# Kernel optimization log

Measured on AMD Instinct MI355X. Metric: run time of the kernel, lower is better.

Reference implementation:

```python
import jax, jax.numpy as jnp
import numpy as np

N_SRC, N_TGT, K = 16384, 65536, 8      # coarse nodes, fine nodes, IDW neighbours per target
C, C_SKIP, S, HID = 16, 2, 32, 64      # mv channels (d_model), skip mv channels, scalars, MLP hidden
MV = 16                                # PGA multivector blade dimension


def setup_inputs() -> dict:
    key = jax.random.key(0)
    ks = jax.random.split(key, 11)
    E = N_TGT * K
    return {
        'mv_src': jax.random.normal(ks[0], (N_SRC, C, MV), jnp.float32),
        'mv_skip': jax.random.normal(ks[1], (N_TGT, C_SKIP, MV), jnp.float32),
        'sc_src': jax.random.normal(ks[2], (N_SRC, S), jnp.float32),
        'sc_skip': jax.random.normal(ks[3], (N_TGT, S), jnp.float32),
        'pos_src': jax.random.uniform(ks[4], (N_SRC, 3), jnp.float32),
        'pos_tgt': jax.random.uniform(ks[5], (N_TGT, 3), jnp.float32),
        'interp_source': jax.random.randint(ks[6], (E,), 0, N_SRC, dtype=jnp.int32),
        # every target receives exactly K source contributions (sorted, like torch_geometric knn edges)
        'interp_target': jnp.repeat(jnp.arange(N_TGT, dtype=jnp.int32), K),
        'W1_mv': jax.random.normal(ks[7], (C + C_SKIP, HID), jnp.float32) / np.float32(np.sqrt(C + C_SKIP)),
        'W2_mv': jax.random.normal(ks[8], (HID, C), jnp.float32) / np.float32(np.sqrt(HID)),
        'W1_s': jax.random.normal(ks[9], (2 * S, HID), jnp.float32) / np.float32(np.sqrt(2 * S)),
        'b1_s': jnp.zeros((HID,), jnp.float32),
        'W2_s': jax.random.normal(ks[10], (HID, S), jnp.float32) / np.float32(np.sqrt(HID)),
        'b2_s': jnp.zeros((S,), jnp.float32),
    }


def _interp(mv_src, mv_skip, sc_src, sc_skip, pos_src, pos_tgt,
            interp_source, interp_target, W1_mv, W2_mv, W1_s, b1_s, W2_s, b2_s):
    # --- inverse-distance-weighted interpolation (gather -> weight -> scatter-sum) ---
    pos_diff = pos_src[interp_source] - pos_tgt[interp_target]            # [E,3]
    d2 = jnp.clip(jnp.sum(pos_diff * pos_diff, axis=-1), 1e-16)           # [E]
    w = 1.0 / d2                                                          # IDW weight
    denom = jax.ops.segment_sum(w, interp_target, num_segments=N_TGT)     # [N_tgt]
    mv = jax.ops.segment_sum(mv_src[interp_source] * w[:, None, None],
                             interp_target, num_segments=N_TGT) / denom[:, None, None]
    sc = jax.ops.segment_sum(sc_src[interp_source] * w[:, None],
                             interp_target, num_segments=N_TGT) / denom[:, None]
    # --- skip concat (torch.cat dim=-2 for multivectors, dim=-1 for scalars) ---
    mv = jnp.concatenate((mv, mv_skip), axis=-2)                          # [N_tgt, C+C_SKIP, 16]
    sc = jnp.concatenate((sc, sc_skip), axis=-1)                          # [N_tgt, 2S]
    # --- equivariant MLP: channel-mixing linear on multivectors (blade-wise), gated scalar path ---
    mv_h = jnp.einsum('nci,ch->nhi', mv, W1_mv)                           # [N_tgt, HID, 16]
    sc_h = jax.nn.gelu(sc @ W1_s + b1_s)                                  # [N_tgt, HID]
    mv_o = jnp.einsum('nhi,hc->nci', mv_h, W2_mv)                         # [N_tgt, C, 16]
    sc_o = sc_h @ W2_s + b2_s                                             # [N_tgt, S]
    return mv_o, sc_o


def reference(mv_src, mv_skip, sc_src, sc_skip, pos_src, pos_tgt,
              interp_source, interp_target, W1_mv, W2_mv, W1_s, b1_s, W2_s, b2_s):
    return _interp(mv_src, mv_skip, sc_src, sc_skip, pos_src, pos_tgt,
                   interp_source, interp_target, W1_mv, W2_mv, W1_s, b1_s, W2_s, b2_s)
```

## Files before the change

kernel.cpp:

```cpp
#include <hip/hip_runtime.h>

#define N_SRC 16384
#define N_TGT 65536
#define KNN 8
#define CMV 16
#define CSKIP 2
#define SSC 32
#define HID 64
#define MVD 16

#define OUT_MV_ELEMS (N_TGT * CMV * MVD)
#define PROJ_OFFSET 512

__device__ __forceinline__ float gelu_tanh(float x) {
    const float k0 = 0.7978845608028654f;
    const float k1 = 0.044715f;
    float y = k0 * fmaf(k1 * x, x * x * x >= 0.f ? x * x : x * x, x);
    (void)y;
    float yy = k0 * (x + k1 * x * x * x);
    return 0.5f * x * (1.0f + tanhf(yy));
}

__global__ __launch_bounds__(256) void kA_preproject(
        const float* __restrict__ mv_src,
        const float* __restrict__ W1_mv,
        const float* __restrict__ W2_mv,
        float* __restrict__ ws) {
    __shared__ float sWeff[CMV][MVD];
    int tid = threadIdx.x;
    {
        int c = tid >> 4, d = tid & 15;
        float a = 0.f;
        #pragma unroll 8
        for (int h = 0; h < HID; ++h)
            a = fmaf(W1_mv[c * HID + h], W2_mv[h * MVD + d], a);
        sWeff[c][d] = a;
    }
    if (blockIdx.x == 0 && tid < 32) {
        int j = tid >> 4, d = tid & 15;
        float a = 0.f;
        #pragma unroll 8
        for (int h = 0; h < HID; ++h)
            a = fmaf(W1_mv[(CMV + j) * HID + h], W2_mv[h * MVD + d], a);
        ws[j * MVD + d] = a;
    }
    __syncthreads();

    int lane = tid & 63;
    int d = lane >> 2, q = lane & 3;
    float wcol[CMV];
    #pragma unroll
    for (int c = 0; c < CMV; ++c) wcol[c] = sWeff[c][d];

    float* proj = ws + PROJ_OFFSET;
    int wid = (int)((blockIdx.x * blockDim.x + tid) >> 6);
    int nw  = (int)((gridDim.x * blockDim.x) >> 6);
    for (int s = wid; s < N_SRC; s += nw) {
        const float* row = mv_src + (size_t)s * 256;
        float4 o = make_float4(0.f, 0.f, 0.f, 0.f);
        #pragma unroll
        for (int c = 0; c < CMV; ++c) {
            float4 v = *(const float4*)(row + c * 16 + q * 4);
            o.x = fmaf(v.x, wcol[c], o.x);
            o.y = fmaf(v.y, wcol[c], o.y);
            o.z = fmaf(v.z, wcol[c], o.z);
            o.w = fmaf(v.w, wcol[c], o.w);
        }
        *(float4*)(proj + (size_t)s * 256 + lane * 4) = o;
    }
}

__global__ __launch_bounds__(256) void kB_mv(
        const float* __restrict__ ws,
        const float* __restrict__ mv_skip,
        const float* __restrict__ pos_src,
        const float* __restrict__ pos_tgt,
        const int*   __restrict__ isrc,
        float* __restrict__ out) {
    int tid = threadIdx.x;
    int lane = tid & 63;
    int d = lane >> 2, q = lane & 3;
    float wsk0 = ws[d];
    float wsk1 = ws[MVD + d];
    const float* proj = ws + PROJ_OFFSET;

    int wid = (int)((blockIdx.x * blockDim.x + tid) >> 6);
    int nw  = (int)((gridDim.x * blockDim.x) >> 6);
    for (int t = wid; t < N_TGT; t += nw) {
        float w = 0.f; int src = 0;
        if (lane < KNN) {
            src = isrc[t * KNN + lane];
            float dx = pos_src[src * 3 + 0] - pos_tgt[t * 3 + 0];
            float dy = pos_src[src * 3 + 1] - pos_tgt[t * 3 + 1];
            float dz = pos_src[src * 3 + 2] - pos_tgt[t * 3 + 2];
            float d2 = fmaxf(dx * dx + dy * dy + dz * dz, 1e-16f);
            w = 1.0f / d2;
        }
        float denom = w;
        denom += __shfl_xor(denom, 1);
        denom += __shfl_xor(denom, 2);
        denom += __shfl_xor(denom, 4);
        denom = __shfl(denom, 0);
        float invd = 1.0f / denom;

        float4 acc = make_float4(0.f, 0.f, 0.f, 0.f);
        #pragma unroll
        for (int k = 0; k < KNN; ++k) {
            int   sk = __builtin_amdgcn_readlane(src, k);
            float wk = __uint_as_float(__builtin_amdgcn_readlane(__float_as_uint(w), k));
            float4 v = *(const float4*)(proj + (size_t)sk * 256 + lane * 4);
            acc.x = fmaf(wk, v.x, acc.x);
            acc.y = fmaf(wk, v.y, acc.y);
            acc.z = fmaf(wk, v.z, acc.z);
            acc.w = fmaf(wk, v.w, acc.w);
        }
        const float4 u0 = *(const float4*)(mv_skip + (size_t)t * 32 + q * 4);
        const float4 u1 = *(const float4*)(mv_skip + (size_t)t * 32 + 16 + q * 4);
        float4 o;
        o.x = fmaf(acc.x, invd, fmaf(wsk0, u0.x, wsk1 * u1.x));
        o.y = fmaf(acc.y, invd, fmaf(wsk0, u0.y, wsk1 * u1.y));
        o.z = fmaf(acc.z, invd, fmaf(wsk0, u0.z, wsk1 * u1.z));
        o.w = fmaf(acc.w, invd, fmaf(wsk0, u0.w, wsk1 * u1.w));
        *(float4*)(out + (size_t)t * 256 + lane * 4) = o;
    }
}

__global__ __launch_bounds__(256) void kBf_mv(
        const float* __restrict__ mv_src,
        const float* __restrict__ mv_skip,
        const float* __restrict__ pos_src,
        const float* __restrict__ pos_tgt,
        const int*   __restrict__ isrc,
        const float* __restrict__ W1_mv,
        const float* __restrict__ W2_mv,
        float* __restrict__ out) {
    __shared__ float sWeff[CMV + CSKIP][MVD];
    __shared__ float stage[4][256];
    int tid = threadIdx.x;
    for (int e = tid; e < (CMV + CSKIP) * MVD; e += 256) {
        int c = e >> 4, d = e & 15;
        float a = 0.f;
        #pragma unroll 8
        for (int h = 0; h < HID; ++h)
            a = fmaf(W1_mv[c * HID + h], W2_mv[h * MVD + d], a);
        sWeff[c][d] = a;
    }
    __syncthreads();

    int lane = tid & 63, wv = tid >> 6;
    int d = lane >> 2, q = lane & 3;
    float wcol[CMV + CSKIP];
    #pragma unroll
    for (int c = 0; c < CMV + CSKIP; ++c) wcol[c] = sWeff[c][d];

    int wid = (int)((blockIdx.x * blockDim.x + tid) >> 6);
    int nw  = (int)((gridDim.x * blockDim.x) >> 6);
    for (int t = wid; t < N_TGT; t += nw) {
        float w = 0.f; int src = 0;
        if (lane < KNN) {
            src = isrc[t * KNN + lane];
            float dx = pos_src[src * 3 + 0] - pos_tgt[t * 3 + 0];
            float dy = pos_src[src * 3 + 1] - pos_tgt[t * 3 + 1];
            float dz = pos_src[src * 3 + 2] - pos_tgt[t * 3 + 2];
            float d2 = fmaxf(dx * dx + dy * dy + dz * dz, 1e-16f);
            w = 1.0f / d2;
        }
        float denom = w;
        denom += __shfl_xor(denom, 1);
        denom += __shfl_xor(denom, 2);
        denom += __shfl_xor(denom, 4);
        denom = __shfl(denom, 0);
        float invd = 1.0f / denom;

        float4 acc = make_float4(0.f, 0.f, 0.f, 0.f);
        #pragma unroll
        for (int k = 0; k < KNN; ++k) {
            int   sk = __builtin_amdgcn_readlane(src, k);
            float wk = __uint_as_float(__builtin_amdgcn_readlane(__float_as_uint(w), k));
            float4 v = *(const float4*)(mv_src + (size_t)sk * 256 + lane * 4);
            acc.x = fmaf(wk, v.x, acc.x);
            acc.y = fmaf(wk, v.y, acc.y);
            acc.z = fmaf(wk, v.z, acc.z);
            acc.w = fmaf(wk, v.w, acc.w);
        }
        asm volatile("" ::: "memory");
        *(float4*)&stage[wv][lane * 4] = acc;
        asm volatile("s_waitcnt lgkmcnt(0)" ::: "memory");
        __builtin_amdgcn_sched_barrier(0);

        float4 o = make_float4(0.f, 0.f, 0.f, 0.f);
        #pragma unroll
        for (int c = 0; c < CMV; ++c) {
            float4 v = *(const float4*)&stage[wv][c * 16 + q * 4];
            o.x = fmaf(v.x, wcol[c], o.x);
            o.y = fmaf(v.y, wcol[c], o.y);
            o.z = fmaf(v.z, wcol[c], o.z);
            o.w = fmaf(v.w, wcol[c], o.w);
        }
        const float4 u0 = *(const float4*)(mv_skip + (size_t)t * 32 + q * 4);
        const float4 u1 = *(const float4*)(mv_skip + (size_t)t * 32 + 16 + q * 4);
        float4 r;
        r.x = fmaf(o.x, invd, fmaf(wcol[16], u0.x, wcol[17] * u1.x));
        r.y = fmaf(o.y, invd, fmaf(wcol[16], u0.y, wcol[17] * u1.y));
        r.z = fmaf(o.z, invd, fmaf(wcol[16], u0.z, wcol[17] * u1.z));
        r.w = fmaf(o.w, invd, fmaf(wcol[16], u0.w, wcol[17] * u1.w));
        *(float4*)(out + (size_t)t * 256 + lane * 4) = r;
    }
}

__global__ __launch_bounds__(256) void kC_scalar(
        const float* __restrict__ sc_src,
        const float* __restrict__ sc_skip,
        const float* __restrict__ pos_src,
        const float* __restrict__ pos_tgt,
        const int*   __restrict__ isrc,
        const float* __restrict__ W1_s,
        const float* __restrict__ b1_s,
        const float* __restrict__ W2_s,
        const float* __restrict__ b2_s,
        float* __restrict__ out) {
    __shared__ float sW1[HID * HID];
    __shared__ float sW2T[SSC][68];
    __shared__ float sXT[HID][64];
    __shared__ float sH[64][68];
    __shared__ float swgt[64][9];
    __shared__ int   ssrcl[64][9];
    __shared__ float sb1[HID], sb2[SSC];

    int tid = threadIdx.x;
    #pragma unroll
    for (int r = 0; r < 4; ++r) {
        float4 v = *(const float4*)(W1_s + (r * 256 + tid) * 4);
        *(float4*)&sW1[(r * 256 + tid) * 4] = v;
    }
    for (int e = tid; e < HID * SSC; e += 256) {
        int h = e >> 5, s = e & 31;
        sW2T[s][h] = W2_s[e];
    }
    if (tid < HID) sb1[tid] = b1_s[tid];
    else if (tid < HID + SSC) sb2[tid - HID] = b2_s[tid - HID];

    int t0 = blockIdx.x * 64;
    if (tid < 64) {
        int t = t0 + tid;
        float ptx = pos_tgt[t * 3 + 0], pty = pos_tgt[t * 3 + 1], ptz = pos_tgt[t * 3 + 2];
        int4 e0 = *(const int4*)(isrc + t * KNN);
        int4 e1 = *(const int4*)(isrc + t * KNN + 4);
        int sk[KNN] = {e0.x, e0.y, e0.z, e0.w, e1.x, e1.y, e1.z, e1.w};
        float wk[KNN];
        float denom = 0.f;
        #pragma unroll
        for (int k = 0; k < KNN; ++k) {
            int s = sk[k];
            float dx = pos_src[s * 3 + 0] - ptx;
            float dy = pos_src[s * 3 + 1] - pty;
            float dz = pos_src[s * 3 + 2] - ptz;
            float d2 = fmaxf(dx * dx + dy * dy + dz * dz, 1e-16f);
            wk[k] = 1.0f / d2;
            denom += wk[k];
        }
        float invd = 1.0f / denom;
        #pragma unroll
        for (int k = 0; k < KNN; ++k) {
            swgt[tid][k] = wk[k] * invd;
            ssrcl[tid][k] = sk[k];
        }
    }
    __syncthreads();

    {
        int tl = tid & 63;
        int part = tid >> 6;
        float cat[16];
        if (part < 2) {
            #pragma unroll
            for (int i = 0; i < 16; ++i) cat[i] = 0.f;
            #pragma unroll
            for (int k = 0; k < KNN; ++k) {
                float wn = swgt[tl][k];
                const float* row = sc_src + (size_t)ssrcl[tl][k] * SSC + part * 16;
                #pragma unroll
                for (int i4 = 0; i4 < 4; ++i4) {
                    float4 v = *(const float4*)(row + i4 * 4);
                    cat[i4 * 4 + 0] = fmaf(wn, v.x, cat[i4 * 4 + 0]);
                    cat[i4 * 4 + 1] = fmaf(wn, v.y, cat[i4 * 4 + 1]);
                    cat[i4 * 4 + 2] = fmaf(wn, v.z, cat[i4 * 4 + 2]);
                    cat[i4 * 4 + 3] = fmaf(wn, v.w, cat[i4 * 4 + 3]);
                }
            }
        } else {
            const float* row = sc_skip + (size_t)(t0 + tl) * SSC + (part - 2) * 16;
            #pragma unroll
            for (int i4 = 0; i4 < 4; ++i4) {
                float4 v = *(const float4*)(row + i4 * 4);
                cat[i4 * 4 + 0] = v.x; cat[i4 * 4 + 1] = v.y;
                cat[i4 * 4 + 2] = v.z; cat[i4 * 4 + 3] = v.w;
            }
        }
        #pragma unroll
        for (int i = 0; i < 16; ++i)
            sXT[part * 16 + i][tl] = cat[i];
    }
    __syncthreads();

    int wv = tid >> 6;
    int lane = tid & 63;
    int tr4 = lane >> 4;
    int hc  = lane & 15;
    int tbase = wv * 16 + tr4 * 4;
    float acc[4][4];
    #pragma unroll
    for (int i = 0; i < 4; ++i)
        #pragma unroll
        for (int j = 0; j < 4; ++j) acc[i][j] = 0.f;

    #pragma unroll 2
    for (int c = 0; c < HID; ++c) {
        float4 xv = *(const float4*)&sXT[c][tbase];
        float4 wv4 = *(const float4*)&sW1[c * HID + hc * 4];
        acc[0][0] = fmaf(xv.x, wv4.x, acc[0][0]);
        acc[0][1] = fmaf(xv.x, wv4.y, acc[0][1]);
        acc[0][2] = fmaf(xv.x, wv4.z, acc[0][2]);
        acc[0][3] = fmaf(xv.x, wv4.w, acc[0][3]);
        acc[1][0] = fmaf(xv.y, wv4.x, acc[1][0]);
        acc[1][1] = fmaf(xv.y, wv4.y, acc[1][1]);
        acc[1][2] = fmaf(xv.y, wv4.z, acc[1][2]);
        acc[1][3] = fmaf(xv.y, wv4.w, acc[1][3]);
        acc[2][0] = fmaf(xv.z, wv4.x, acc[2][0]);
        acc[2][1] = fmaf(xv.z, wv4.y, acc[2][1]);
        acc[2][2] = fmaf(xv.z, wv4.z, acc[2][2]);
        acc[2][3] = fmaf(xv.z, wv4.w, acc[2][3]);
        acc[3][0] = fmaf(xv.w, wv4.x, acc[3][0]);
        acc[3][1] = fmaf(xv.w, wv4.y, acc[3][1]);
        acc[3][2] = fmaf(xv.w, wv4.z, acc[3][2]);
        acc[3][3] = fmaf(xv.w, wv4.w, acc[3][3]);
    }
    {
        float b0 = sb1[hc * 4 + 0], b1 = sb1[hc * 4 + 1];
        float b2 = sb1[hc * 4 + 2], b3 = sb1[hc * 4 + 3];
        #pragma unroll
        for (int i = 0; i < 4; ++i) {
            float4 hv;
            hv.x = gelu_tanh(acc[i][0] + b0);
            hv.y = gelu_tanh(acc[i][1] + b1);
            hv.z = gelu_tanh(acc[i][2] + b2);
            hv.w = gelu_tanh(acc[i][3] + b3);
            *(float4*)&sH[tbase + i][hc * 4] = hv;
        }
    }
    __syncthreads();

    int sc16 = lane & 15;
    float acc2[4][2];
    #pragma unroll
    for (int i = 0; i < 4; ++i) { acc2[i][0] = 0.f; acc2[i][1] = 0.f; }
    #pragma unroll 2
    for (int hh = 0; hh < 16; ++hh) {
        float4 wa = *(const float4*)&sW2T[sc16 * 2 + 0][hh * 4];
        float4 wb = *(const float4*)&sW2T[sc16 * 2 + 1][hh * 4];
        #pragma unroll
        for (int i = 0; i < 4; ++i) {
            float4 hv = *(const float4*)&sH[tbase + i][hh * 4];
            acc2[i][0] = fmaf(hv.x, wa.x, acc2[i][0]);
            acc2[i][0] = fmaf(hv.y, wa.y, acc2[i][0]);
            acc2[i][0] = fmaf(hv.z, wa.z, acc2[i][0]);
            acc2[i][0] = fmaf(hv.w, wa.w, acc2[i][0]);
            acc2[i][1] = fmaf(hv.x, wb.x, acc2[i][1]);
            acc2[i][1] = fmaf(hv.y, wb.y, acc2[i][1]);
            acc2[i][1] = fmaf(hv.z, wb.z, acc2[i][1]);
            acc2[i][1] = fmaf(hv.w, wb.w, acc2[i][1]);
        }
    }
    float* osc = out + OUT_MV_ELEMS;
    float bb0 = sb2[sc16 * 2 + 0], bb1 = sb2[sc16 * 2 + 1];
    #pragma unroll
    for (int i = 0; i < 4; ++i) {
        int t = t0 + tbase + i;
        float2 r = make_float2(acc2[i][0] + bb0, acc2[i][1] + bb1);
        *(float2*)&osc[(size_t)t * SSC + sc16 * 2] = r;
    }
}

extern "C" void kernel_launch(void* const* d_in, const int* in_sizes, int n_in,
                              void* d_out, int out_size, void* d_ws, size_t ws_size,
                              hipStream_t stream) {
    const float* mv_src   = (const float*)d_in[0];
    const float* mv_skip  = (const float*)d_in[1];
    const float* sc_src   = (const float*)d_in[2];
    const float* sc_skip  = (const float*)d_in[3];
    const float* pos_src  = (const float*)d_in[4];
    const float* pos_tgt  = (const float*)d_in[5];
    const int*   isrc     = (const int*)d_in[6];
    const float* W1_mv    = (const float*)d_in[8];
    const float* W2_mv    = (const float*)d_in[9];
    const float* W1_s     = (const float*)d_in[10];
    const float* b1_s     = (const float*)d_in[11];
    const float* W2_s     = (const float*)d_in[12];
    const float* b2_s     = (const float*)d_in[13];
    float* out = (float*)d_out;
    float* ws  = (float*)d_ws;

    size_t need_ws_bytes = (size_t)(PROJ_OFFSET + (size_t)N_SRC * 256) * sizeof(float);
    if (ws_size >= need_ws_bytes) {
        hipLaunchKernelGGL(kA_preproject, dim3(512), dim3(256), 0, stream,
                           mv_src, W1_mv, W2_mv, ws);
        hipLaunchKernelGGL(kB_mv, dim3(2048), dim3(256), 0, stream,
                           ws, mv_skip, pos_src, pos_tgt, isrc, out);
    } else {
        hipLaunchKernelGGL(kBf_mv, dim3(2048), dim3(256), 0, stream,
                           mv_src, mv_skip, pos_src, pos_tgt, isrc, W1_mv, W2_mv, out);
    }
    hipLaunchKernelGGL(kC_scalar, dim3(N_TGT / 64), dim3(256), 0, stream,
                       sc_src, sc_skip, pos_src, pos_tgt, isrc,
                       W1_s, b1_s, W2_s, b2_s, out);
}
```

Measured before the change: 234.7 us.

## Batch 8 targets per wave and gather sources in phase order for L2 locality

Measured after the change: 238.4 us. About the same (+1.6%).

```diff
diff --git a/kernel.cpp b/kernel.cpp
--- a/kernel.cpp
+++ b/kernel.cpp
@@ -12,11 +12,12 @@
 #define OUT_MV_ELEMS (N_TGT * CMV * MVD)
 #define PROJ_OFFSET 512
 
+#define NPHASE 8
+#define PSHIFT 11
+
 __device__ __forceinline__ float gelu_tanh(float x) {
     const float k0 = 0.7978845608028654f;
     const float k1 = 0.044715f;
-    float y = k0 * fmaf(k1 * x, x * x * x >= 0.f ? x * x : x * x, x);
-    (void)y;
     float yy = k0 * (x + k1 * x * x * x);
     return 0.5f * x * (1.0f + tanhf(yy));
 }
@@ -85,42 +86,64 @@
     const float* proj = ws + PROJ_OFFSET;
 
     int wid = (int)((blockIdx.x * blockDim.x + tid) >> 6);
-    int nw  = (int)((gridDim.x * blockDim.x) >> 6);
-    for (int t = wid; t < N_TGT; t += nw) {
-        float w = 0.f; int src = 0;
+    int t0 = wid * 8;
+
+    int   srcv[8];
+    float wnv[8];
+    #pragma unroll
+    for (int tl = 0; tl < 8; ++tl) {
+        int t = t0 + tl;
+        float w = 0.f; int s = 0;
         if (lane < KNN) {
-            src = isrc[t * KNN + lane];
-            float dx = pos_src[src * 3 + 0] - pos_tgt[t * 3 + 0];
-            float dy = pos_src[src * 3 + 1] - pos_tgt[t * 3 + 1];
-            float dz = pos_src[src * 3 + 2] - pos_tgt[t * 3 + 2];
+            s = isrc[t * KNN + lane];
+            float dx = pos_src[s * 3 + 0] - pos_tgt[t * 3 + 0];
+            float dy = pos_src[s * 3 + 1] - pos_tgt[t * 3 + 1];
+            float dz = pos_src[s * 3 + 2] - pos_tgt[t * 3 + 2];
             float d2 = fmaxf(dx * dx + dy * dy + dz * dz, 1e-16f);
             w = 1.0f / d2;
         }
-        float denom = w;
-        denom += __shfl_xor(denom, 1);
-        denom += __shfl_xor(denom, 2);
-        denom += __shfl_xor(denom, 4);
-        denom = __shfl(denom, 0);
-        float invd = 1.0f / denom;
-
-        float4 acc = make_float4(0.f, 0.f, 0.f, 0.f);
-        #pragma unroll
-        for (int k = 0; k < KNN; ++k) {
-            int   sk = __builtin_amdgcn_readlane(src, k);
-            float wk = __uint_as_float(__builtin_amdgcn_readlane(__float_as_uint(w), k));
-            float4 v = *(const float4*)(proj + (size_t)sk * 256 + lane * 4);
-            acc.x = fmaf(wk, v.x, acc.x);
-            acc.y = fmaf(wk, v.y, acc.y);
-            acc.z = fmaf(wk, v.z, acc.z);
-            acc.w = fmaf(wk, v.w, acc.w);
-        }
+        float den = w;
+        den += __shfl_xor(den, 1);
+        den += __shfl_xor(den, 2);
+        den += __shfl_xor(den, 4);
+        srcv[tl] = s;
+        wnv[tl]  = w / den;
+    }
+
+    float4 acc[8];
+    #pragma unroll
+    for (int tl = 0; tl < 8; ++tl) acc[tl] = make_float4(0.f, 0.f, 0.f, 0.f);
+
+    for (int p = 0; p < NPHASE; ++p) {
+        #pragma unroll
+        for (int tl = 0; tl < 8; ++tl) {
+            unsigned long long m =
+                __ballot((lane < KNN) && ((srcv[tl] >> PSHIFT) == p));
+            while (m) {
+                int k = __builtin_ctzll(m);
+                m &= m - 1;
+                int   sk = __builtin_amdgcn_readlane(srcv[tl], k);
+                float wk = __uint_as_float(
+                    __builtin_amdgcn_readlane(__float_as_uint(wnv[tl]), k));
+                const float4 v = *(const float4*)(proj + (size_t)sk * 256 + lane * 4);
+                acc[tl].x = fmaf(wk, v.x, acc[tl].x);
+                acc[tl].y = fmaf(wk, v.y, acc[tl].y);
+                acc[tl].z = fmaf(wk, v.z, acc[tl].z);
+                acc[tl].w = fmaf(wk, v.w, acc[tl].w);
+            }
+        }
+    }
+
+    #pragma unroll
+    for (int tl = 0; tl < 8; ++tl) {
+        int t = t0 + tl;
         const float4 u0 = *(const float4*)(mv_skip + (size_t)t * 32 + q * 4);
         const float4 u1 = *(const float4*)(mv_skip + (size_t)t * 32 + 16 + q * 4);
         float4 o;
-        o.x = fmaf(acc.x, invd, fmaf(wsk0, u0.x, wsk1 * u1.x));
-        o.y = fmaf(acc.y, invd, fmaf(wsk0, u0.y, wsk1 * u1.y));
-        o.z = fmaf(acc.z, invd, fmaf(wsk0, u0.z, wsk1 * u1.z));
-        o.w = fmaf(acc.w, invd, fmaf(wsk0, u0.w, wsk1 * u1.w));
+        o.x = acc[tl].x + fmaf(wsk0, u0.x, wsk1 * u1.x);
+        o.y = acc[tl].y + fmaf(wsk0, u0.y, wsk1 * u1.y);
+        o.z = acc[tl].z + fmaf(wsk0, u0.z, wsk1 * u1.z);
+        o.w = acc[tl].w + fmaf(wsk0, u0.w, wsk1 * u1.w);
         *(float4*)(out + (size_t)t * 256 + lane * 4) = o;
     }
 }
```

## Store pre-projected source multivectors in fp16 and batch target gathers

Applied to the files above, without the earlier changes.

Measured after the change: 208.6 us. -11.1%, faster.

```diff
diff --git a/kernel.cpp b/kernel.cpp
--- a/kernel.cpp
+++ b/kernel.cpp
@@ -1,4 +1,5 @@
 #include <hip/hip_runtime.h>
+#include <hip/hip_fp16.h>
 
 #define N_SRC 16384
 #define N_TGT 65536
@@ -15,8 +16,6 @@
 __device__ __forceinline__ float gelu_tanh(float x) {
     const float k0 = 0.7978845608028654f;
     const float k1 = 0.044715f;
-    float y = k0 * fmaf(k1 * x, x * x * x >= 0.f ? x * x : x * x, x);
-    (void)y;
     float yy = k0 * (x + k1 * x * x * x);
     return 0.5f * x * (1.0f + tanhf(yy));
 }
@@ -52,7 +51,7 @@
     #pragma unroll
     for (int c = 0; c < CMV; ++c) wcol[c] = sWeff[c][d];
 
-    float* proj = ws + PROJ_OFFSET;
+    __half* proj = (__half*)(ws + PROJ_OFFSET);
     int wid = (int)((blockIdx.x * blockDim.x + tid) >> 6);
     int nw  = (int)((gridDim.x * blockDim.x) >> 6);
     for (int s = wid; s < N_SRC; s += nw) {
@@ -66,11 +65,14 @@
             o.z = fmaf(v.z, wcol[c], o.z);
             o.w = fmaf(v.w, wcol[c], o.w);
         }
-        *(float4*)(proj + (size_t)s * 256 + lane * 4) = o;
-    }
-}
-
-__global__ __launch_bounds__(256) void kB_mv(
+        union { __half2 h[2]; uint2 u; } P;
+        P.h[0] = __floats2half2_rn(o.x, o.y);
+        P.h[1] = __floats2half2_rn(o.z, o.w);
+        *(uint2*)(proj + (size_t)s * 256 + lane * 4) = P.u;
+    }
+}
+
+__global__ __launch_bounds__(256, 6) void kB_mv(
         const float* __restrict__ ws,
         const float* __restrict__ mv_skip,
         const float* __restrict__ pos_src,
@@ -82,46 +84,94 @@
     int d = lane >> 2, q = lane & 3;
     float wsk0 = ws[d];
     float wsk1 = ws[MVD + d];
-    const float* proj = ws + PROJ_OFFSET;
+    const __half* proj = (const __half*)(ws + PROJ_OFFSET);
 
     int wid = (int)((blockIdx.x * blockDim.x + tid) >> 6);
-    int nw  = (int)((gridDim.x * blockDim.x) >> 6);
-    for (int t = wid; t < N_TGT; t += nw) {
-        float w = 0.f; int src = 0;
+    int t0 = wid * 8;
+
+    #pragma unroll
+    for (int pp = 0; pp < 4; ++pp) {
+        int tA = t0 + pp * 2, tB = tA + 1;
+        float wA = 0.f, wB = 0.f; int sA = 0, sB = 0;
         if (lane < KNN) {
-            src = isrc[t * KNN + lane];
-            float dx = pos_src[src * 3 + 0] - pos_tgt[t * 3 + 0];
-            float dy = pos_src[src * 3 + 1] - pos_tgt[t * 3 + 1];
-            float dz = pos_src[src * 3 + 2] - pos_tgt[t * 3 + 2];
-            float d2 = fmaxf(dx * dx + dy * dy + dz * dz, 1e-16f);
-            w = 1.0f / d2;
-        }
-        float denom = w;
-        denom += __shfl_xor(denom, 1);
-        denom += __shfl_xor(denom, 2);
-        denom += __shfl_xor(denom, 4);
-        denom = __shfl(denom, 0);
-        float invd = 1.0f / denom;
-
-        float4 acc = make_float4(0.f, 0.f, 0.f, 0.f);
-        #pragma unroll
-        for (int k = 0; k < KNN; ++k) {
-            int   sk = __builtin_amdgcn_readlane(src, k);
-            float wk = __uint_as_float(__builtin_amdgcn_readlane(__float_as_uint(w), k));
-            float4 v = *(const float4*)(proj + (size_t)sk * 256 + lane * 4);
-            acc.x = fmaf(wk, v.x, acc.x);
-            acc.y = fmaf(wk, v.y, acc.y);
-            acc.z = fmaf(wk, v.z, acc.z);
-            acc.w = fmaf(wk, v.w, acc.w);
-        }
-        const float4 u0 = *(const float4*)(mv_skip + (size_t)t * 32 + q * 4);
-        const float4 u1 = *(const float4*)(mv_skip + (size_t)t * 32 + 16 + q * 4);
-        float4 o;
-        o.x = fmaf(acc.x, invd, fmaf(wsk0, u0.x, wsk1 * u1.x));
-        o.y = fmaf(acc.y, invd, fmaf(wsk0, u0.y, wsk1 * u1.y));
-        o.z = fmaf(acc.z, invd, fmaf(wsk0, u0.z, wsk1 * u1.z));
-        o.w = fmaf(acc.w, invd, fmaf(wsk0, u0.w, wsk1 * u1.w));
-        *(float4*)(out + (size_t)t * 256 + lane * 4) = o;
+            sA = isrc[tA * KNN + lane];
+            sB = isrc[tB * KNN + lane];
+            float ax = pos_src[sA * 3 + 0] - pos_tgt[tA * 3 + 0];
+            float ay = pos_src[sA * 3 + 1] - pos_tgt[tA * 3 + 1];
+            float az = pos_src[sA * 3 + 2] - pos_tgt[tA * 3 + 2];
+            float bx = pos_src[sB * 3 + 0] - pos_tgt[tB * 3 + 0];
+            float by = pos_src[sB * 3 + 1] - pos_tgt[tB * 3 + 1];
+            float bz = pos_src[sB * 3 + 2] - pos_tgt[tB * 3 + 2];
+            float dA = fmaxf(ax * ax + ay * ay + az * az, 1e-16f);
+            float dB = fmaxf(bx * bx + by * by + bz * bz, 1e-16f);
+            wA = 1.0f / dA;
+            wB = 1.0f / dB;
+        }
+        float denA = wA, denB = wB;
+        denA += __shfl_xor(denA, 1); denB += __shfl_xor(denB, 1);
+        denA += __shfl_xor(denA, 2); denB += __shfl_xor(denB, 2);
+        denA += __shfl_xor(denA, 4); denB += __shfl_xor(denB, 4);
+        float wnA = wA / denA, wnB = wB / denB;
+
+        uint2 g[16];
+        #pragma unroll
+        for (int k = 0; k < KNN; ++k) {
+            int sk = __builtin_amdgcn_readlane(sA, k);
+            g[k] = *(const uint2*)(proj + (size_t)sk * 256 + lane * 4);
+        }
+        #pragma unroll
+        for (int k = 0; k < KNN; ++k) {
+            int sk = __builtin_amdgcn_readlane(sB, k);
+            g[8 + k] = *(const uint2*)(proj + (size_t)sk * 256 + lane * 4);
+        }
+
+        float4 accA = make_float4(0.f, 0.f, 0.f, 0.f);
+        float4 accB = make_float4(0.f, 0.f, 0.f, 0.f);
+        #pragma unroll
+        for (int k = 0; k < KNN; ++k) {
+            float wk = __uint_as_float(
+                __builtin_amdgcn_readlane(__float_as_uint(wnA), k));
+            union { uint2 u; __half2 h[2]; } P; P.u = g[k];
+            float2 lo = __half22float2(P.h[0]);
+            float2 hi = __half22float2(P.h[1]);
+            accA.x = fmaf(wk, lo.x, accA.x);
+            accA.y = fmaf(wk, lo.y, accA.y);
+            accA.z = fmaf(wk, hi.x, accA.z);
+            accA.w = fmaf(wk, hi.y, accA.w);
+        }
+        #pragma unroll
+        for (int k = 0; k < KNN; ++k) {
+            float wk = __uint_as_float(
+                __builtin_amdgcn_readlane(__float_as_uint(wnB), k));
+            union { uint2 u; __half2 h[2]; } P; P.u = g[8 + k];
+            float2 lo = __half22float2(P.h[0]);
+            float2 hi = __half22float2(P.h[1]);
+            accB.x = fmaf(wk, lo.x, accB.x);
+            accB.y = fmaf(wk, lo.y, accB.y);
+            accB.z = fmaf(wk, hi.x, accB.z);
+            accB.w = fmaf(wk, hi.y, accB.w);
+        }
+
+        {
+            const float4 u0 = *(const float4*)(mv_skip + (size_t)tA * 32 + q * 4);
+            const float4 u1 = *(const float4*)(mv_skip + (size_t)tA * 32 + 16 + q * 4);
+            float4 o;
+            o.x = accA.x + fmaf(wsk0, u0.x, wsk1 * u1.x);
+            o.y = accA.y + fmaf(wsk0, u0.y, wsk1 * u1.y);
+            o.z = accA.z + fmaf(wsk0, u0.z, wsk1 * u1.z);
+            o.w = accA.w + fmaf(wsk0, u0.w, wsk1 * u1.w);
+            *(float4*)(out + (size_t)tA * 256 + lane * 4) = o;
+        }
+        {
+            const float4 u0 = *(const float4*)(mv_skip + (size_t)tB * 32 + q * 4);
+            const float4 u1 = *(const float4*)(mv_skip + (size_t)tB * 32 + 16 + q * 4);
+            float4 o;
+            o.x = accB.x + fmaf(wsk0, u0.x, wsk1 * u1.x);
+            o.y = accB.y + fmaf(wsk0, u0.y, wsk1 * u1.y);
+            o.z = accB.z + fmaf(wsk0, u0.z, wsk1 * u1.z);
+            o.w = accB.w + fmaf(wsk0, u0.w, wsk1 * u1.w);
+            *(float4*)(out + (size_t)tB * 256 + lane * 4) = o;
+        }
     }
 }
 
@@ -221,7 +271,7 @@
         float* __restrict__ out) {
     __shared__ float sW1[HID * HID];
     __shared__ float sW2T[SSC][68];
-    __shared__ float sXT[HID][64];
+    __shared__ float sXT[HID][68];
     __shared__ float sH[64][68];
     __shared__ float swgt[64][9];
     __shared__ int   ssrcl[64][9];
@@ -269,37 +319,47 @@
     __syncthreads();
 
     {
-        int tl = tid & 63;
-        int part = tid >> 6;
-        float cat[16];
-        if (part < 2) {
+        int wv = tid >> 6, lane = tid & 63;
+        int k = lane >> 3;
+        int m = lane & 7;
+        for (int i = 0; i < 16; i += 4) {
+            int tb = wv * 16 + i;
+            float4 v[4]; float wn4[4];
             #pragma unroll
-            for (int i = 0; i < 16; ++i) cat[i] = 0.f;
+            for (int j = 0; j < 4; ++j) {
+                int tl = tb + j;
+                wn4[j] = swgt[tl][k];
+                int sk = ssrcl[tl][k];
+                v[j] = *(const float4*)(sc_src + (size_t)sk * SSC + m * 4);
+            }
+            float4 u;
+            if (lane < 32)
+                u = *(const float4*)(sc_skip + (size_t)(t0 + tb + k) * SSC + m * 4);
             #pragma unroll
-            for (int k = 0; k < KNN; ++k) {
-                float wn = swgt[tl][k];
-                const float* row = sc_src + (size_t)ssrcl[tl][k] * SSC + part * 16;
+            for (int j = 0; j < 4; ++j) {
+                float4 a = v[j]; float wn = wn4[j];
+                a.x *= wn; a.y *= wn; a.z *= wn; a.w *= wn;
                 #pragma unroll
-                for (int i4 = 0; i4 < 4; ++i4) {
-                    float4 v = *(const float4*)(row + i4 * 4);
-                    cat[i4 * 4 + 0] = fmaf(wn, v.x, cat[i4 * 4 + 0]);
-                    cat[i4 * 4 + 1] = fmaf(wn, v.y, cat[i4 * 4 + 1]);
-                    cat[i4 * 4 + 2] = fmaf(wn, v.z, cat[i4 * 4 + 2]);
-                    cat[i4 * 4 + 3] = fmaf(wn, v.w, cat[i4 * 4 + 3]);
+                for (int sft = 8; sft <= 32; sft <<= 1) {
+                    a.x += __shfl_xor(a.x, sft);
+                    a.y += __shfl_xor(a.y, sft);
+                    a.z += __shfl_xor(a.z, sft);
+                    a.w += __shfl_xor(a.w, sft);
+                }
+                if (lane < 8) {
+                    sXT[4 * lane + 0][tb + j] = a.x;
+                    sXT[4 * lane + 1][tb + j] = a.y;
+                    sXT[4 * lane + 2][tb + j] = a.z;
+                    sXT[4 * lane + 3][tb + j] = a.w;
                 }
             }
-        } else {
-            const float* row = sc_skip + (size_t)(t0 + tl) * SSC + (part - 2) * 16;
-            #pragma unroll
-            for (int i4 = 0; i4 < 4; ++i4) {
-                float4 v = *(const float4*)(row + i4 * 4);
-                cat[i4 * 4 + 0] = v.x; cat[i4 * 4 + 1] = v.y;
-                cat[i4 * 4 + 2] = v.z; cat[i4 * 4 + 3] = v.w;
+            if (lane < 32) {
+                sXT[SSC + 4 * m + 0][tb + k] = u.x;
+                sXT[SSC + 4 * m + 1][tb + k] = u.y;
+                sXT[SSC + 4 * m + 2][tb + k] = u.z;
+                sXT[SSC + 4 * m + 3][tb + k] = u.w;
             }
         }
-        #pragma unroll
-        for (int i = 0; i < 16; ++i)
-            sXT[part * 16 + i][tl] = cat[i];
     }
     __syncthreads();
 
@@ -400,7 +460,7 @@
     float* out = (float*)d_out;
     float* ws  = (float*)d_ws;
 
-    size_t need_ws_bytes = (size_t)(PROJ_OFFSET + (size_t)N_SRC * 256) * sizeof(float);
+    size_t need_ws_bytes = PROJ_OFFSET * sizeof(float) + (size_t)N_SRC * 256 * sizeof(__half);
     if (ws_size >= need_ws_bytes) {
         hipLaunchKernelGGL(kA_preproject, dim3(512), dim3(256), 0, stream,
                            mv_src, W1_mv, W2_mv, ws);
```
